# Optimization experiments

Hardware: AMD Instinct MI355X
Metric: run time of the kernel (lower is better)

## Reference

```python
import jax, jax.numpy as jnp
import numpy as np

N = 100000
E = 1600000
DIM = 128
HID = 16
HEADS = 4
NUM_CLASSES = 2
NEG_SLOPE = 0.2


def _glorot(key, shape):
    fan_in, fan_out = shape[0], shape[-1]
    lim = jnp.sqrt(6.0 / (fan_in + fan_out))
    return jax.random.uniform(key, shape, jnp.float32, -lim, lim)


def setup_inputs() -> dict:
    key = jax.random.key(0)
    ks = jax.random.split(key, 12)
    x = jax.random.normal(ks[0], (N, DIM), jnp.float32)
    edge_index = jax.random.randint(ks[1], (2, E), 0, N, jnp.int32)
    # conv1: in=DIM, out=HID, heads=HEADS
    W1 = _glorot(ks[2], (DIM, HEADS * HID))
    att_src1 = _glorot(ks[3], (HEADS, HID))
    att_dst1 = _glorot(ks[4], (HEADS, HID))
    b1 = jnp.zeros((HEADS * HID,), jnp.float32)
    # conv2: in=HEADS*HID, out=NUM_CLASSES, heads=1
    W2 = _glorot(ks[5], (HEADS * HID, NUM_CLASSES))
    att_src2 = _glorot(ks[6], (1, NUM_CLASSES))
    att_dst2 = _glorot(ks[7], (1, NUM_CLASSES))
    b2 = jnp.zeros((NUM_CLASSES,), jnp.float32)
    return {"x": x, "edge_index": edge_index, "W1": W1, "att_src1": att_src1,
            "att_dst1": att_dst1, "b1": b1, "W2": W2, "att_src2": att_src2,
            "att_dst2": att_dst2, "b2": b2}


def gat_conv(x, src, dst, W, a_src, a_dst, bias, heads, out_ch):
    n = x.shape[0]
    h = (x @ W).reshape(n, heads, out_ch)                      # [N,H,C]
    alpha_s = jnp.sum(h * a_src[None], axis=-1)                # [N,H]
    alpha_d = jnp.sum(h * a_dst[None], axis=-1)                # [N,H]
    e = alpha_s[src] + alpha_d[dst]                            # [Etot,H]
    e = jnp.where(e > 0, e, NEG_SLOPE * e)                     # leaky_relu
    m = jax.ops.segment_max(e, dst, num_segments=n)            # segment softmax
    e = jnp.exp(e - m[dst])
    s = jax.ops.segment_sum(e, dst, num_segments=n)
    alpha = e / (s[dst] + 1e-16)                               # [Etot,H]
    msg = h[src] * alpha[..., None]                            # [Etot,H,C]
    out = jax.ops.segment_sum(msg, dst, num_segments=n)        # [N,H,C]
    return out.reshape(n, heads * out_ch) + bias


def reference(x, edge_index, W1, att_src1, att_dst1, b1, W2, att_src2, att_dst2, b2):
    n = x.shape[0]
    loops = jnp.arange(n, dtype=edge_index.dtype)
    src = jnp.concatenate([edge_index[0], loops])
    dst = jnp.concatenate([edge_index[1], loops])
    # dropout p=0.6 is identity in eval mode
    h = gat_conv(x, src, dst, W1, att_src1, att_dst1, b1, HEADS, HID)
    h = jax.nn.elu(h)
    out = gat_conv(h, src, dst, W2, att_src2, att_dst2, b2, 1, NUM_CLASSES)
    return out
```

## Files before the change

kernel.cpp:

```cpp
#include <hip/hip_runtime.h>
#include <math.h>


#define NB 256
#define BSH 9
#define SRC_MASK 0x1FFFF
#define KC_CHUNK 4096
#define MAXB 12288

static __device__ __forceinline__ unsigned short f2bf(float f) {
    union { float f; unsigned int u; } v; v.f = f;
    unsigned int r = (v.u + 0x7fffu + ((v.u >> 16) & 1u)) >> 16;
    return (unsigned short)r;
}
static __device__ __forceinline__ float bf2f(unsigned short s) {
    union { unsigned int u; float f; } v; v.u = ((unsigned int)s) << 16;
    return v.f;
}
static __device__ __forceinline__ float lrexp(float raw) {
    return __expf(raw > 0.f ? raw : 0.2f * raw);
}

__global__ __launch_bounds__(256) void k_gemm1(const float* __restrict__ x,
                                               const float* __restrict__ W,
                                               const float* __restrict__ att_s,
                                               const float* __restrict__ att_d,
                                               unsigned short* __restrict__ h1b,
                                               float* __restrict__ as1,
                                               float* __restrict__ ad1, int n) {
    __shared__ float xs[64 * 132];
    __shared__ float Ws[128 * 64];
    const int t = threadIdx.x;
    const int row0 = blockIdx.x * 64;
    for (int i = t; i < 2048; i += 256)
        ((float4*)Ws)[i] = ((const float4*)W)[i];
    for (int i = t; i < 2048; i += 256) {
        int r = i >> 5, k4 = i & 31;
        float4 v = make_float4(0.f, 0.f, 0.f, 0.f);
        if (row0 + r < n) v = ((const float4*)x)[(size_t)(row0 + r) * 32 + k4];
        *(float4*)&xs[r * 132 + k4 * 4] = v;
    }
    __syncthreads();
    const int tx = t & 15, ty = t >> 4;
    float acc[4][4] = {};
    for (int k = 0; k < 128; k += 4) {
        float4 av[4], bv[4];
#pragma unroll
        for (int i = 0; i < 4; ++i) av[i] = *(const float4*)&xs[(ty * 4 + i) * 132 + k];
#pragma unroll
        for (int kk = 0; kk < 4; ++kk) bv[kk] = *(const float4*)&Ws[(k + kk) * 64 + tx * 4];
#pragma unroll
        for (int kk = 0; kk < 4; ++kk) {
            float4 b = bv[kk];
#pragma unroll
            for (int i = 0; i < 4; ++i) {
                float a = ((const float*)&av[i])[kk];
                acc[i][0] += a * b.x; acc[i][1] += a * b.y;
                acc[i][2] += a * b.z; acc[i][3] += a * b.w;
            }
        }
    }
    float4 sv = ((const float4*)att_s)[tx];
    float4 dv = ((const float4*)att_d)[tx];
    float ps[4], pd[4];
#pragma unroll
    for (int i = 0; i < 4; ++i) {
        ps[i] = acc[i][0] * sv.x + acc[i][1] * sv.y + acc[i][2] * sv.z + acc[i][3] * sv.w;
        pd[i] = acc[i][0] * dv.x + acc[i][1] * dv.y + acc[i][2] * dv.z + acc[i][3] * dv.w;
        int r = row0 + ty * 4 + i;
        if (r < n) {
            ushort4 b;
            b.x = f2bf(acc[i][0]); b.y = f2bf(acc[i][1]);
            b.z = f2bf(acc[i][2]); b.w = f2bf(acc[i][3]);
            ((ushort4*)h1b)[(size_t)r * 16 + tx] = b;
        }
    }
    __syncthreads();
    float* redA = xs;
    float* redB = xs + 1024;
#pragma unroll
    for (int i = 0; i < 4; ++i) {
        int row = ty * 4 + i;
        redA[row * 16 + tx] = ps[i];
        redB[row * 16 + tx] = pd[i];
    }
    __syncthreads();
    {
        int row = t >> 2, h = t & 3;
        int r = row0 + row;
        if (r < n) {
            const float* pa = &redA[row * 16 + h * 4];
            const float* pb = &redB[row * 16 + h * 4];
            as1[r * 4 + h] = pa[0] + pa[1] + pa[2] + pa[3];
            ad1[r * 4 + h] = pb[0] + pb[1] + pb[2] + pb[3];
        }
    }
}

__global__ __launch_bounds__(256) void kC_bin(const int* __restrict__ src,
                                              const int* __restrict__ dst,
                                              int* __restrict__ bcursor,
                                              unsigned int* __restrict__ staged, int E) {
    __shared__ unsigned int pairs[KC_CHUNK];
    __shared__ unsigned char binOf[KC_CHUNK];
    __shared__ int h[NB], lofs[NB], lcur[NB], gbase[NB];
    int t = threadIdx.x;
    int base = blockIdx.x * KC_CHUNK;
    int cnt = E - base; if (cnt > KC_CHUNK) cnt = KC_CHUNK;
    h[t] = 0; __syncthreads();
    unsigned int myV[16]; int myBin[16];
#pragma unroll
    for (int k = 0; k < 16; ++k) {
        int li = k * 256 + t;
        myBin[k] = -1;
        if (li < cnt) {
            int gi = base + li;
            int s = src[gi], d = dst[gi];
            int bin = d >> BSH;
            myV[k] = ((unsigned int)(d & ((1 << BSH) - 1)) << 17) | (unsigned int)s;
            myBin[k] = bin;
            atomicAdd(&h[bin], 1);
        }
    }
    __syncthreads();
    int hv = h[t];
    lofs[t] = hv; __syncthreads();
    for (int o = 1; o < NB; o <<= 1) {
        int xv = (t >= o) ? lofs[t - o] : 0;
        __syncthreads();
        lofs[t] += xv; __syncthreads();
    }
    int excl = lofs[t] - hv;
    if (hv) gbase[t] = t * MAXB + atomicAdd(&bcursor[t], hv);
    __syncthreads();
    lofs[t] = excl; lcur[t] = excl;
    __syncthreads();
#pragma unroll
    for (int k = 0; k < 16; ++k) {
        if (myBin[k] >= 0) {
            int p = atomicAdd(&lcur[myBin[k]], 1);
            pairs[p] = myV[k];
            binOf[p] = (unsigned char)myBin[k];
        }
    }
    __syncthreads();
    for (int i = t; i < cnt; i += 256) {
        int b = binOf[i];
        staged[gbase[b] + (i - lofs[b])] = pairs[i];
    }
}

__global__ __launch_bounds__(256) void kD_group(const unsigned int* __restrict__ staged,
                                                const int* __restrict__ bcursor,
                                                unsigned int* __restrict__ grouped,
                                                int* __restrict__ offs,
                                                int* __restrict__ dcnt, int n) {
    __shared__ int lh[512], lofs2[512], lcur2[512];
    __shared__ unsigned int st[MAXB];
    int t = threadIdx.x;
    int b = blockIdx.x;
    int base = b * MAXB;
    int cnt = bcursor[b];
    lh[t] = 0; lh[t + 256] = 0;
    __syncthreads();
    for (int i = t; i < cnt; i += 256)
        atomicAdd(&lh[staged[base + i] >> 17], 1);
    __syncthreads();
    int a0 = lh[2 * t], a1 = lh[2 * t + 1];
    int sp = a0 + a1;
    lcur2[t] = sp; __syncthreads();
    for (int o = 1; o < NB; o <<= 1) {
        int xv = (t >= o) ? lcur2[t - o] : 0;
        __syncthreads();
        lcur2[t] += xv; __syncthreads();
    }
    int excl = lcur2[t] - sp;
    lofs2[2 * t] = excl; lofs2[2 * t + 1] = excl + a0;
    __syncthreads();
#pragma unroll
    for (int q = 0; q < 2; ++q) {
        int dl = t + q * 256;
        int d = (b << BSH) + dl;
        if (d < n) {
            offs[d] = base + lofs2[dl];
            dcnt[d] = lh[dl];
        }
        lcur2[dl] = lofs2[dl];
    }
    __syncthreads();
    for (int i = t; i < cnt; i += 256) {
        unsigned int v = staged[base + i];
        int p = atomicAdd(&lcur2[v >> 17], 1);
        st[p] = v;
    }
    __syncthreads();
    for (int i = t; i < cnt; i += 256)
        grouped[base + i] = st[i];
}

__global__ __launch_bounds__(256) void k_agg1(
        const int* __restrict__ offs, const int* __restrict__ dcnt,
        const unsigned int* __restrict__ grouped,
        const unsigned short* __restrict__ h1b, const float* __restrict__ as1,
        const float* __restrict__ ad1, const float* __restrict__ b1,
        const float* __restrict__ W2,
        const float* __restrict__ att_s2, const float* __restrict__ att_d2,
        float4* __restrict__ pack, int n) {
    const int lane = threadIdx.x & 63;
    const int d = blockIdx.x * 4 + (threadIdx.x >> 6);
    if (d >= n) return;
    const int c = lane;
    const int h = lane >> 4;
    const int sub = lane & 15;
    const int off0 = offs[d];
    const int total = dcnt[d] + 1;
    const float adh = ad1[d * 4 + h];
    const float wselfv = lrexp(as1[d * 4 + h] + adh);

    float acc = 0.f, wsum = 0.f;
    for (int base = 0; base < total; base += 16) {
        int e = base + sub;
        float w = 0.f; int s = d;
        if (e < total) {
            if (e < total - 1) {
                unsigned int v = grouped[off0 + e];
                s = (int)(v & SRC_MASK);
                w = lrexp(as1[s * 4 + h] + adh);
            } else {
                w = wselfv;
            }
        }
        wsum += w;
#pragma unroll
        for (int j = 0; j < 16; ++j) {
            int sj = __builtin_amdgcn_readlane(s, j);
            float wj = __shfl(w, (h << 4) + j);
            acc += wj * bf2f(h1b[(size_t)sj * 64 + c]);
        }
    }
    wsum += __shfl_xor(wsum, 1);
    wsum += __shfl_xor(wsum, 2);
    wsum += __shfl_xor(wsum, 4);
    wsum += __shfl_xor(wsum, 8);
    float o1 = acc / (wsum + 1e-16f) + b1[c];
    float o = o1 > 0.f ? o1 : expm1f(o1);
    float2 wv = ((const float2*)W2)[c];
    float p0 = o * wv.x, p1 = o * wv.y;
#pragma unroll
    for (int m = 1; m < 64; m <<= 1) {
        p0 += __shfl_xor(p0, m);
        p1 += __shfl_xor(p1, m);
    }
    if (lane == 0) {
        pack[d] = make_float4(p0, p1,
                              p0 * att_s2[0] + p1 * att_s2[1],
                              p0 * att_d2[0] + p1 * att_d2[1]);
    }
}

__global__ __launch_bounds__(256) void k_agg2(
        const int* __restrict__ offs, const int* __restrict__ dcnt,
        const unsigned int* __restrict__ grouped,
        const float4* __restrict__ pack, const float* __restrict__ b2,
        float* __restrict__ out, int n) {
    int t = threadIdx.x;
    int g = blockIdx.x * 16 + (t >> 4);
    int sub = t & 15;
    if (g >= n) return;
    int off0 = offs[g];
    int total = dcnt[g] + 1;
    float ad = pack[g].w;
    float a0 = 0.f, a1 = 0.f, ws = 0.f;
    for (int e = sub; e < total; e += 16) {
        int s = (e == total - 1) ? g : (int)(grouped[off0 + e] & SRC_MASK);
        float4 ps = pack[s];
        float w = lrexp(ps.z + ad);
        a0 += w * ps.x; a1 += w * ps.y; ws += w;
    }
#pragma unroll
    for (int m = 1; m < 16; m <<= 1) {
        a0 += __shfl_xor(a0, m);
        a1 += __shfl_xor(a1, m);
        ws += __shfl_xor(ws, m);
    }
    if (sub == 0) {
        float inv = 1.f / (ws + 1e-16f);
        out[(size_t)g * 2 + 0] = a0 * inv + b2[0];
        out[(size_t)g * 2 + 1] = a1 * inv + b2[1];
    }
}

extern "C" void kernel_launch(void* const* d_in, const int* in_sizes, int n_in,
                              void* d_out, int out_size, void* d_ws, size_t ws_size,
                              hipStream_t stream) {
    const float* x    = (const float*)d_in[0];
    const int*   ei   = (const int*)d_in[1];
    const float* W1   = (const float*)d_in[2];
    const float* as1w = (const float*)d_in[3];
    const float* ad1w = (const float*)d_in[4];
    const float* b1   = (const float*)d_in[5];
    const float* W2   = (const float*)d_in[6];
    const float* as2w = (const float*)d_in[7];
    const float* ad2w = (const float*)d_in[8];
    const float* b2   = (const float*)d_in[9];
    const int n = in_sizes[0] / 128;
    const int E = in_sizes[1] / 2;
    float* out = (float*)d_out;

    char* ws = (char*)d_ws;
    size_t off = 0;
    auto alloc = [&](size_t bytes) {
        void* p = ws + off;
        off = (off + bytes + 255) & ~(size_t)255;
        return p;
    };
    unsigned short* h1b = (unsigned short*)alloc((size_t)n * 64 * 2);
    float*  as1    = (float*)alloc((size_t)n * 4 * 4);
    float*  ad1    = (float*)alloc((size_t)n * 4 * 4);
    float4* pack   = (float4*)alloc((size_t)n * 16);
    int*    offs   = (int*)alloc((size_t)n * 4);
    int*    dcnt   = (int*)alloc((size_t)n * 4);
    int*    bcursor= (int*)alloc(NB * 4);
    unsigned int* staged  = (unsigned int*)alloc((size_t)NB * MAXB * 4);
    unsigned int* grouped = (unsigned int*)alloc((size_t)NB * MAXB * 4);

    hipMemsetAsync(bcursor, 0, NB * 4, stream);

    const int nblk = (E + KC_CHUNK - 1) / KC_CHUNK;
    const int nbk = (n + 511) >> 9;
    k_gemm1<<<(n + 63) / 64, 256, 0, stream>>>(x, W1, as1w, ad1w, h1b, as1, ad1, n);
    kC_bin<<<nblk, 256, 0, stream>>>(ei, ei + E, bcursor, staged, E);
    kD_group<<<nbk, 256, 0, stream>>>(staged, bcursor, grouped, offs, dcnt, n);
    k_agg1<<<(n + 3) / 4, 256, 0, stream>>>(offs, dcnt, grouped, h1b, as1, ad1,
                                            b1, W2, as2w, ad2w, pack, n);
    k_agg2<<<(n + 15) / 16, 256, 0, stream>>>(offs, dcnt, grouped, pack, b2, out, n);
}
```

Baseline: 246.7 us.

## Prefetch edge indices in agg1, hoist self-loops, fold memset into gemm

Several changes land together. The bcursor memset launch is replaced by zeroing inside k_gemm1 block 0. The binning chunk shrinks to 2048 edges with 8 per thread and a smaller MAXB, which gives more blocks. k_agg1 software-pipelines the next batch of grouped index and attention-score loads ahead of the gather loop. Both aggregation kernels handle the self-loop term outside the edge loop, and expm1f is swapped for __expf-1. The risks are that MAXB=9216 could overflow a bin, and that zeroing bcursor relies on k_gemm1 finishing before kC_bin, which holds because both run in order on the same stream.

```diff
diff --git a/kernel.cpp b/kernel.cpp
--- a/kernel.cpp
+++ b/kernel.cpp
@@ -5,8 +5,9 @@
 #define NB 256
 #define BSH 9
 #define SRC_MASK 0x1FFFF
-#define KC_CHUNK 4096
-#define MAXB 12288
+#define KC_CHUNK 2048
+#define KC_PT 8
+#define MAXB 9216
 
 static __device__ __forceinline__ unsigned short f2bf(float f) {
     union { float f; unsigned int u; } v; v.f = f;
@@ -27,11 +28,13 @@
                                                const float* __restrict__ att_d,
                                                unsigned short* __restrict__ h1b,
                                                float* __restrict__ as1,
-                                               float* __restrict__ ad1, int n) {
+                                               float* __restrict__ ad1,
+                                               int* __restrict__ bcursor, int n) {
     __shared__ float xs[64 * 132];
     __shared__ float Ws[128 * 64];
     const int t = threadIdx.x;
     const int row0 = blockIdx.x * 64;
+    if (blockIdx.x == 0) bcursor[t] = 0;
     for (int i = t; i < 2048; i += 256)
         ((float4*)Ws)[i] = ((const float4*)W)[i];
     for (int i = t; i < 2048; i += 256) {
@@ -108,9 +111,9 @@
     int base = blockIdx.x * KC_CHUNK;
     int cnt = E - base; if (cnt > KC_CHUNK) cnt = KC_CHUNK;
     h[t] = 0; __syncthreads();
-    unsigned int myV[16]; int myBin[16];
-#pragma unroll
-    for (int k = 0; k < 16; ++k) {
+    unsigned int myV[KC_PT]; int myBin[KC_PT];
+#pragma unroll
+    for (int k = 0; k < KC_PT; ++k) {
         int li = k * 256 + t;
         myBin[k] = -1;
         if (li < cnt) {
@@ -136,7 +139,7 @@
     lofs[t] = excl; lcur[t] = excl;
     __syncthreads();
 #pragma unroll
-    for (int k = 0; k < 16; ++k) {
+    for (int k = 0; k < KC_PT; ++k) {
         if (myBin[k] >= 0) {
             int p = atomicAdd(&lcur[myBin[k]], 1);
             pairs[p] = myV[k];
@@ -213,37 +216,48 @@
     const int h = lane >> 4;
     const int sub = lane & 15;
     const int off0 = offs[d];
-    const int total = dcnt[d] + 1;
+    const int total = dcnt[d];
     const float adh = ad1[d * 4 + h];
     const float wselfv = lrexp(as1[d * 4 + h] + adh);
 
-    float acc = 0.f, wsum = 0.f;
+    float acc = wselfv * bf2f(h1b[(size_t)d * 64 + c]);
+    float wsum = 0.f;
+
+    int s_cur = d; float a_cur = 0.f; bool v_ok = (sub < total);
+    if (v_ok) {
+        unsigned int v = grouped[off0 + sub];
+        s_cur = (int)(v & SRC_MASK);
+        a_cur = as1[s_cur * 4 + h];
+    }
     for (int base = 0; base < total; base += 16) {
-        int e = base + sub;
-        float w = 0.f; int s = d;
-        if (e < total) {
-            if (e < total - 1) {
-                unsigned int v = grouped[off0 + e];
-                s = (int)(v & SRC_MASK);
-                w = lrexp(as1[s * 4 + h] + adh);
-            } else {
-                w = wselfv;
-            }
-        }
+        int en = base + 16 + sub;
+        bool n_ok = (en < total);
+        unsigned int v_n = 0;
+        if (n_ok) v_n = grouped[off0 + en];
+
+        float w = v_ok ? lrexp(a_cur + adh) : 0.f;
         wsum += w;
+        int s = s_cur;
 #pragma unroll
         for (int j = 0; j < 16; ++j) {
             int sj = __builtin_amdgcn_readlane(s, j);
             float wj = __shfl(w, (h << 4) + j);
             acc += wj * bf2f(h1b[(size_t)sj * 64 + c]);
         }
+        int s_n = d; float a_n = 0.f;
+        if (n_ok) {
+            s_n = (int)(v_n & SRC_MASK);
+            a_n = as1[s_n * 4 + h];
+        }
+        s_cur = s_n; a_cur = a_n; v_ok = n_ok;
     }
     wsum += __shfl_xor(wsum, 1);
     wsum += __shfl_xor(wsum, 2);
     wsum += __shfl_xor(wsum, 4);
     wsum += __shfl_xor(wsum, 8);
+    wsum += wselfv;
     float o1 = acc / (wsum + 1e-16f) + b1[c];
-    float o = o1 > 0.f ? o1 : expm1f(o1);
+    float o = o1 > 0.f ? o1 : (__expf(o1) - 1.f);
     float2 wv = ((const float2*)W2)[c];
     float p0 = o * wv.x, p1 = o * wv.y;
 #pragma unroll
@@ -268,11 +282,16 @@
     int sub = t & 15;
     if (g >= n) return;
     int off0 = offs[g];
-    int total = dcnt[g] + 1;
-    float ad = pack[g].w;
+    int total = dcnt[g];
+    float4 pg = pack[g];
+    float ad = pg.w;
     float a0 = 0.f, a1 = 0.f, ws = 0.f;
+    if (sub == 0) {
+        float w = lrexp(pg.z + ad);
+        a0 = w * pg.x; a1 = w * pg.y; ws = w;
+    }
     for (int e = sub; e < total; e += 16) {
-        int s = (e == total - 1) ? g : (int)(grouped[off0 + e] & SRC_MASK);
+        int s = (int)(grouped[off0 + e] & SRC_MASK);
         float4 ps = pack[s];
         float w = lrexp(ps.z + ad);
         a0 += w * ps.x; a1 += w * ps.y; ws += w;
@@ -324,11 +343,10 @@
     unsigned int* staged  = (unsigned int*)alloc((size_t)NB * MAXB * 4);
     unsigned int* grouped = (unsigned int*)alloc((size_t)NB * MAXB * 4);
 
-    hipMemsetAsync(bcursor, 0, NB * 4, stream);
-
     const int nblk = (E + KC_CHUNK - 1) / KC_CHUNK;
     const int nbk = (n + 511) >> 9;
-    k_gemm1<<<(n + 63) / 64, 256, 0, stream>>>(x, W1, as1w, ad1w, h1b, as1, ad1, n);
+    k_gemm1<<<(n + 63) / 64, 256, 0, stream>>>(x, W1, as1w, ad1w, h1b, as1, ad1,
+                                               bcursor, n);
     kC_bin<<<nblk, 256, 0, stream>>>(ei, ei + E, bcursor, staged, E);
     kD_group<<<nbk, 256, 0, stream>>>(staged, bcursor, grouped, offs, dcnt, n);
     k_agg1<<<(n + 3) / 4, 256, 0, stream>>>(offs, dcnt, grouped, h1b, as1, ad1,
```

Measured after the change: 241.0 us. 2.3% less time.
